# Performance work log

Measured on AMD Instinct MI355X. Metric: run time of the kernel, lower is better.

## Reference

```python
import jax, jax.numpy as jnp
import numpy as np

K = 3
PAD = K // 2
EPS = 1e-5


def setup_inputs() -> dict:
    key = jax.random.key(0)
    k1, k2, k3 = jax.random.split(key, 3)
    B, C, H, W = 16, 256, 56, 56
    x = jax.random.normal(k1, (B, C, H, W), jnp.float32)
    offset = jax.random.normal(k2, (B, 2 * K * K, H, W), jnp.float32)  # matches torch.randn offsets
    weight = jax.random.normal(k3, (C, C, K, K), jnp.float32) * (1.0 / np.sqrt(C * K * K))
    gamma = jnp.ones((C,), jnp.float32)
    beta = jnp.zeros((C,), jnp.float32)
    return {"x": x, "offset": offset, "weight": weight, "gamma": gamma, "beta": beta}


def _bilinear_sample(x, py, px):
    # x: [B,C,H,W]; py,px: [B,H,W] fractional sample coords; zero padding outside.
    B, C, H, W = x.shape
    y0 = jnp.floor(py)
    x0 = jnp.floor(px)
    wy1 = py - y0  # weight for y0+1
    wx1 = px - x0
    wy0 = 1.0 - wy1
    wx0 = 1.0 - wx1
    x_flat = x.reshape(B, C, H * W)

    def corner(yc, xc, w):
        valid = ((yc >= 0) & (yc <= H - 1) & (xc >= 0) & (xc <= W - 1)).astype(x.dtype)
        yi = jnp.clip(yc, 0, H - 1).astype(jnp.int32)
        xi = jnp.clip(xc, 0, W - 1).astype(jnp.int32)
        idx = (yi * W + xi).reshape(B, 1, H * W)
        v = jnp.take_along_axis(x_flat, jnp.broadcast_to(idx, (B, C, H * W)), axis=2)
        return v.reshape(B, C, H, W) * (w * valid)[:, None, :, :]

    return (corner(y0, x0, wy0 * wx0) + corner(y0, x0 + 1, wy0 * wx1)
            + corner(y0 + 1, x0, wy1 * wx0) + corner(y0 + 1, x0 + 1, wy1 * wx1))


def _deform_conv(x, offset, weight):
    B, C, H, W = x.shape
    base_y = jnp.arange(H, dtype=x.dtype)[None, :, None]  # [1,H,1]
    base_x = jnp.arange(W, dtype=x.dtype)[None, None, :]  # [1,1,W]
    out = jnp.zeros((B, weight.shape[0], H, W), x.dtype)
    for k in range(K * K):  # fixed small loop over kernel taps
        kh, kw = k // K, k % K
        py = base_y + (kh - PAD) + offset[:, 2 * k]
        px = base_x + (kw - PAD) + offset[:, 2 * k + 1]
        samp = _bilinear_sample(x, py, px)  # [B,C,H,W]
        out = out + jnp.einsum('bchw,oc->bohw', samp, weight[:, :, kh, kw])
    return out


def reference(x, offset, weight, gamma, beta):
    y = _deform_conv(x, offset, weight)
    mean = y.mean(axis=(0, 2, 3))
    var = y.var(axis=(0, 2, 3))  # biased var, training-mode BN
    yhat = (y - mean[:, None, None]) * jax.lax.rsqrt(var[:, None, None] + EPS)
    return jax.nn.relu(yhat * gamma[:, None, None] + beta[:, None, None])
```

## Files before the change

kernel.cpp:

```cpp
#include <hip/hip_runtime.h>
#include <stdint.h>

#define HW    3136
#define CH    256
#define NBAT  16
#define RDIM  2304
#define NPOS  50176
#define EPSV  1e-5f
#define NCOL  1568

typedef __bf16 bf16x8 __attribute__((ext_vector_type(8)));
typedef float  f32x4  __attribute__((ext_vector_type(4)));
typedef unsigned int u32x4 __attribute__((ext_vector_type(4)));

__device__ __forceinline__ unsigned short f2bf(float f) {
    union { float f; unsigned int u; } z; z.f = f;
    unsigned int u = z.u;
    u += 0x7FFFu + ((u >> 16) & 1u);
    return (unsigned short)(u >> 16);
}

__device__ __forceinline__ unsigned int cvtpk(float lo, float hi) {
    unsigned int r;
    asm("v_cvt_pk_bf16_f32 %0, %1, %2" : "=v"(r) : "v"(lo), "v"(hi));
    return r;
}

__device__ __forceinline__ void gload_lds16(const void* g, void* l) {
    __builtin_amdgcn_global_load_lds(
        (const __attribute__((address_space(1))) unsigned int*)g,
        (__attribute__((address_space(3))) unsigned int*)l,
        16, 0, 0);
}

__global__ __launch_bounds__(256) void k_transpose(const float* __restrict__ x,
                                                   unsigned short* __restrict__ xt) {
    __shared__ float tile[64][65];
    int hw0 = blockIdx.x * 64;
    int c0  = blockIdx.y * 64;
    int b   = blockIdx.z;
    int tx = threadIdx.x & 63;
    int ty = threadIdx.x >> 6;
    const float* xp = x + ((size_t)(b * CH + c0)) * HW + hw0;
#pragma unroll
    for (int i = 0; i < 16; i++) {
        int c_l = ty + i * 4;
        tile[c_l][tx] = xp[(size_t)c_l * HW + tx];
    }
    __syncthreads();
    unsigned short* op = xt + ((size_t)(b * HW + hw0)) * CH + c0;
#pragma unroll
    for (int i = 0; i < 16; i++) {
        int hw_l = ty + i * 4;
        op[(size_t)hw_l * CH + tx] = f2bf(tile[tx][hw_l]);
    }
}

__global__ __launch_bounds__(256) void k_w2(const float* __restrict__ w,
                                            unsigned short* __restrict__ w2) {
    int idx = blockIdx.x * 256 + threadIdx.x;
    int c = idx & 255;
    int k = (idx >> 8) % 9;
    int o = idx / RDIM;
    w2[idx] = f2bf(w[o * RDIM + c * 9 + k]);
}

#define BK 64
__global__ __launch_bounds__(512, 4) void k_fgemm(const unsigned short* __restrict__ xt,
                                                  const float* __restrict__ off,
                                                  const unsigned short* __restrict__ W2,
                                                  float* __restrict__ y,
                                                  float* __restrict__ psum_s,
                                                  float* __restrict__ psum_q) {
    __shared__ __align__(16) unsigned short lA[256 * BK];
    __shared__ __align__(16) unsigned short lB[64 * BK];
    int t    = threadIdx.x;
    int wid  = t >> 6;
    int lane = t & 63;

    int bid  = blockIdx.x;
    int xcd  = bid & 7;
    int j    = bid >> 3;
    int b    = 2 * xcd + (j >= 49 ? 1 : 0);
    int spat = (j >= 49) ? j - 49 : j;
    int n0   = spat * 64;
    const unsigned short* xb = xt + (size_t)b * HW * CH;

    int m_off = (wid >> 1) * 64;
    int n_off = (wid & 1) * 32;
    int fr = lane & 15;
    int fq = lane >> 4;

    int bp  = t >> 3;
    int bcg = t & 7;
    int hw = n0 + bp;
    int h = hw / 56, w = hw - h * 56;
    unsigned short* lbdst = &lB[bp * BK + ((bcg ^ (bp & 7)) * 8)];

    f32x4 acc[4][2];
#pragma unroll
    for (int m = 0; m < 4; m++)
#pragma unroll
        for (int n = 0; n < 2; n++)
            acc[m][n] = (f32x4){0.f, 0.f, 0.f, 0.f};

    for (int tap = 0; tap < 9; tap++) {
        int   cidx[4];
        float cwgt[4];
        {
            float offY = off[((size_t)(b * 18 + 2 * tap)) * HW + hw];
            float offX = off[((size_t)(b * 18 + 2 * tap + 1)) * HW + hw];
            float py = (float)(h + tap / 3 - 1) + offY;
            float px = (float)(w + tap % 3 - 1) + offX;
            float y0f = floorf(py), x0f = floorf(px);
            float fy = py - y0f, fx = px - x0f;
            float wy[2] = {1.f - fy, fy};
            float wx[2] = {1.f - fx, fx};
#pragma unroll
            for (int jj = 0; jj < 4; jj++) {
                int dy = jj >> 1, dx = jj & 1;
                float ycf = y0f + (float)dy, xcf = x0f + (float)dx;
                bool v = (ycf >= 0.f) && (ycf <= 55.f) && (xcf >= 0.f) && (xcf <= 55.f);
                int yi = min(max((int)ycf, 0), 55);
                int xi = min(max((int)xcf, 0), 55);
                cidx[jj] = yi * 56 + xi;
                cwgt[jj] = v ? wy[dy] * wx[dx] : 0.f;
            }
        }

#pragma unroll
        for (int kk4 = 0; kk4 < 4; kk4++) {
            int r0 = tap * 256 + kk4 * 64;
            int c0 = kk4 * 64 + bcg * 8;
            u32x4 cv0 = *(const u32x4*)(xb + (size_t)cidx[0] * CH + c0);
            u32x4 cv1 = *(const u32x4*)(xb + (size_t)cidx[1] * CH + c0);
            u32x4 cv2 = *(const u32x4*)(xb + (size_t)cidx[2] * CH + c0);
            u32x4 cv3 = *(const u32x4*)(xb + (size_t)cidx[3] * CH + c0);
#pragma unroll
            for (int i = 0; i < 4; i++) {
                int q = t + 512 * i;
                int row = q >> 3;
                int part = (q & 7) ^ (row & 7);
                gload_lds16(W2 + (size_t)row * RDIM + r0 + part * 8,
                            &lA[(size_t)(wid * 64 + 512 * i) * 8]);
            }
            {
                float al[4] = {0.f, 0.f, 0.f, 0.f};
                float ah[4] = {0.f, 0.f, 0.f, 0.f};
#pragma unroll
                for (int i = 0; i < 4; i++) {
                    float w0 = cwgt[0], w1 = cwgt[1], w2v = cwgt[2], w3 = cwgt[3];
                    al[i] = fmaf(w0, __uint_as_float(cv0[i] << 16),
                            fmaf(w1, __uint_as_float(cv1[i] << 16),
                            fmaf(w2v, __uint_as_float(cv2[i] << 16),
                                 w3 * __uint_as_float(cv3[i] << 16))));
                    ah[i] = fmaf(w0, __uint_as_float(cv0[i] & 0xffff0000u),
                            fmaf(w1, __uint_as_float(cv1[i] & 0xffff0000u),
                            fmaf(w2v, __uint_as_float(cv2[i] & 0xffff0000u),
                                 w3 * __uint_as_float(cv3[i] & 0xffff0000u))));
                }
                u32x4 ov;
#pragma unroll
                for (int i = 0; i < 4; i++) ov[i] = cvtpk(al[i], ah[i]);
                *(u32x4*)lbdst = ov;
            }
            __syncthreads();
            __builtin_amdgcn_s_setprio(1);
#pragma unroll
            for (int kk = 0; kk < 2; kk++) {
                bf16x8 afr[4], bfr[2];
#pragma unroll
                for (int m = 0; m < 4; m++) {
                    int row = m_off + m * 16 + fr;
                    int slot = (kk * 4 + fq) ^ (row & 7);
                    afr[m] = *(const bf16x8*)&lA[row * BK + slot * 8];
                }
#pragma unroll
                for (int n = 0; n < 2; n++) {
                    int row = n_off + n * 16 + fr;
                    int slot = (kk * 4 + fq) ^ (row & 7);
                    bfr[n] = *(const bf16x8*)&lB[row * BK + slot * 8];
                }
#pragma unroll
                for (int m = 0; m < 4; m++)
#pragma unroll
                    for (int n = 0; n < 2; n++)
                        acc[m][n] = __builtin_amdgcn_mfma_f32_16x16x32_bf16(afr[m], bfr[n], acc[m][n], 0, 0, 0);
            }
            __builtin_amdgcn_s_setprio(0);
            __syncthreads();
        }
    }

    float* yb = y + (size_t)b * CH * HW;
#pragma unroll
    for (int m = 0; m < 4; m++) {
        int o = m_off + m * 16 + fq * 4;
#pragma unroll
        for (int n = 0; n < 2; n++) {
            int p = n0 + n_off + n * 16 + fr;
#pragma unroll
            for (int jj = 0; jj < 4; jj++)
                yb[(size_t)(o + jj) * HW + p] = acc[m][n][jj];
        }
    }

    int blk2 = (b * 49 + spat) * 2 + (wid & 1);
#pragma unroll
    for (int m = 0; m < 4; m++)
#pragma unroll
        for (int jj = 0; jj < 4; jj++) {
            float s = acc[m][0][jj] + acc[m][1][jj];
            float q = acc[m][0][jj] * acc[m][0][jj] + acc[m][1][jj] * acc[m][1][jj];
#pragma unroll
            for (int msk = 1; msk < 16; msk <<= 1) {
                s += __shfl_xor(s, msk);
                q += __shfl_xor(q, msk);
            }
            if (fr == 0) {
                int o = m_off + m * 16 + fq * 4 + jj;
                psum_s[(size_t)o * NCOL + blk2] = s;
                psum_q[(size_t)o * NCOL + blk2] = q;
            }
        }
}

__global__ __launch_bounds__(256) void k_stats2(const float* __restrict__ psum_s,
                                                const float* __restrict__ psum_q,
                                                const float* __restrict__ gamma,
                                                const float* __restrict__ beta,
                                                float* __restrict__ scaleArr,
                                                float* __restrict__ shiftArr) {
    int o = blockIdx.x;
    int t = threadIdx.x;
    float s = 0.f, q = 0.f;
    for (int i = t; i < NCOL; i += 256) {
        s += psum_s[(size_t)o * NCOL + i];
        q += psum_q[(size_t)o * NCOL + i];
    }
    __shared__ float r1[256], r2[256];
    r1[t] = s; r2[t] = q;
    __syncthreads();
    for (int st = 128; st > 0; st >>= 1) {
        if (t < st) { r1[t] += r1[t + st]; r2[t] += r2[t + st]; }
        __syncthreads();
    }
    if (t == 0) {
        float inv = 1.f / (float)NPOS;
        float mean = r1[0] * inv;
        float var  = r2[0] * inv - mean * mean;
        float sc = gamma[o] * rsqrtf(var + EPSV);
        scaleArr[o] = sc;
        shiftArr[o] = beta[o] - mean * sc;
    }
}

__global__ __launch_bounds__(256) void k_norm(float* __restrict__ y,
                                              const float* __restrict__ scaleArr,
                                              const float* __restrict__ shiftArr) {
    const int total4 = NBAT * CH * (HW / 4);
    for (int i = blockIdx.x * 256 + threadIdx.x; i < total4; i += gridDim.x * 256) {
        int o = (i / (HW / 4)) & 255;
        float sc = scaleArr[o], sh = shiftArr[o];
        float4 v = ((const float4*)y)[i];
        float4 r;
        r.x = fmaxf(v.x * sc + sh, 0.f);
        r.y = fmaxf(v.y * sc + sh, 0.f);
        r.z = fmaxf(v.z * sc + sh, 0.f);
        r.w = fmaxf(v.w * sc + sh, 0.f);
        ((float4*)y)[i] = r;
    }
}

extern "C" void kernel_launch(void* const* d_in, const int* in_sizes, int n_in,
                              void* d_out, int out_size, void* d_ws, size_t ws_size,
                              hipStream_t stream) {
    const float* x     = (const float*)d_in[0];
    const float* off   = (const float*)d_in[1];
    const float* wgt   = (const float*)d_in[2];
    const float* gamma = (const float*)d_in[3];
    const float* beta  = (const float*)d_in[4];
    float* out = (float*)d_out;
    char* ws = (char*)d_ws;

    unsigned short* W2 = (unsigned short*)(ws + 0);
    unsigned short* xt = (unsigned short*)(ws + 1179648);
    float* psum_s      = (float*)(ws + 26869760);
    float* psum_q      = (float*)(ws + 28475392);
    float* scaleArr    = (float*)(ws + 30081024);
    float* shiftArr    = (float*)(ws + 30082048);

    k_transpose<<<dim3(49, 4, 16), 256, 0, stream>>>(x, xt);
    k_w2<<<2304, 256, 0, stream>>>(wgt, W2);
    k_fgemm<<<784, 512, 0, stream>>>(xt, off, W2, out, psum_s, psum_q);
    k_stats2<<<256, 256, 0, stream>>>(psum_s, psum_q, gamma, beta, scaleArr, shiftArr);
    k_norm<<<2048, 256, 0, stream>>>(out, scaleArr, shiftArr);
}
```

Measured before the change: 167.8 us.

## Double-buffer LDS tiles and prefetch gathers/offsets one K-step ahead in fused deform GEMM

Converts the fused deformable-conv GEMM main loop into a software-pipelined two-stage schedule. The A (weight) and B (bilinear-sampled activation) LDS tiles are double-buffered. The next step's corner gathers and weight staging are issued before the current MFMA block, and the next tap's offsets are prefetched a tap early. This overlaps global gather latency with matrix math and removes one barrier per step, at the cost of doubling LDS use (80KB per block), which can limit the requested 4 blocks per CU and raise register pressure.

```diff
diff --git a/kernel.cpp b/kernel.cpp
--- a/kernel.cpp
+++ b/kernel.cpp
@@ -72,8 +72,8 @@
                                                   float* __restrict__ y,
                                                   float* __restrict__ psum_s,
                                                   float* __restrict__ psum_q) {
-    __shared__ __align__(16) unsigned short lA[256 * BK];
-    __shared__ __align__(16) unsigned short lB[64 * BK];
+    __shared__ __align__(16) unsigned short lA[2][256 * BK];
+    __shared__ __align__(16) unsigned short lB[2][64 * BK];
     int t    = threadIdx.x;
     int wid  = t >> 6;
     int lane = t & 63;
@@ -95,7 +95,7 @@
     int bcg = t & 7;
     int hw = n0 + bp;
     int h = hw / 56, w = hw - h * 56;
-    unsigned short* lbdst = &lB[bp * BK + ((bcg ^ (bp & 7)) * 8)];
+    int lboff = bp * BK + ((bcg ^ (bp & 7)) * 8);
 
     f32x4 acc[4][2];
 #pragma unroll
@@ -104,92 +104,129 @@
         for (int n = 0; n < 2; n++)
             acc[m][n] = (f32x4){0.f, 0.f, 0.f, 0.f};
 
-    for (int tap = 0; tap < 9; tap++) {
-        int   cidx[4];
-        float cwgt[4];
-        {
-            float offY = off[((size_t)(b * 18 + 2 * tap)) * HW + hw];
-            float offX = off[((size_t)(b * 18 + 2 * tap + 1)) * HW + hw];
-            float py = (float)(h + tap / 3 - 1) + offY;
-            float px = (float)(w + tap % 3 - 1) + offX;
-            float y0f = floorf(py), x0f = floorf(px);
-            float fy = py - y0f, fx = px - x0f;
-            float wy[2] = {1.f - fy, fy};
-            float wx[2] = {1.f - fx, fx};
-#pragma unroll
-            for (int jj = 0; jj < 4; jj++) {
-                int dy = jj >> 1, dx = jj & 1;
-                float ycf = y0f + (float)dy, xcf = x0f + (float)dx;
-                bool v = (ycf >= 0.f) && (ycf <= 55.f) && (xcf >= 0.f) && (xcf <= 55.f);
-                int yi = min(max((int)ycf, 0), 55);
-                int xi = min(max((int)xcf, 0), 55);
-                cidx[jj] = yi * 56 + xi;
-                cwgt[jj] = v ? wy[dy] * wx[dx] : 0.f;
-            }
-        }
-
-#pragma unroll
-        for (int kk4 = 0; kk4 < 4; kk4++) {
-            int r0 = tap * 256 + kk4 * 64;
-            int c0 = kk4 * 64 + bcg * 8;
-            u32x4 cv0 = *(const u32x4*)(xb + (size_t)cidx[0] * CH + c0);
-            u32x4 cv1 = *(const u32x4*)(xb + (size_t)cidx[1] * CH + c0);
-            u32x4 cv2 = *(const u32x4*)(xb + (size_t)cidx[2] * CH + c0);
-            u32x4 cv3 = *(const u32x4*)(xb + (size_t)cidx[3] * CH + c0);
-#pragma unroll
-            for (int i = 0; i < 4; i++) {
-                int q = t + 512 * i;
-                int row = q >> 3;
-                int part = (q & 7) ^ (row & 7);
-                gload_lds16(W2 + (size_t)row * RDIM + r0 + part * 8,
-                            &lA[(size_t)(wid * 64 + 512 * i) * 8]);
-            }
-            {
-                float al[4] = {0.f, 0.f, 0.f, 0.f};
-                float ah[4] = {0.f, 0.f, 0.f, 0.f};
-#pragma unroll
-                for (int i = 0; i < 4; i++) {
-                    float w0 = cwgt[0], w1 = cwgt[1], w2v = cwgt[2], w3 = cwgt[3];
-                    al[i] = fmaf(w0, __uint_as_float(cv0[i] << 16),
-                            fmaf(w1, __uint_as_float(cv1[i] << 16),
-                            fmaf(w2v, __uint_as_float(cv2[i] << 16),
-                                 w3 * __uint_as_float(cv3[i] << 16))));
-                    ah[i] = fmaf(w0, __uint_as_float(cv0[i] & 0xffff0000u),
-                            fmaf(w1, __uint_as_float(cv1[i] & 0xffff0000u),
-                            fmaf(w2v, __uint_as_float(cv2[i] & 0xffff0000u),
-                                 w3 * __uint_as_float(cv3[i] & 0xffff0000u))));
+    int   cidx0, cidx1, cidx2, cidx3;
+    float cwgt0, cwgt1, cwgt2, cwgt3;
+    float offYn, offXn;
+
+#define META_COMPUTE(TAP, OY, OX)                                              \
+    {                                                                          \
+        float py = (float)(h + (TAP) / 3 - 1) + (OY);                          \
+        float px = (float)(w + (TAP) % 3 - 1) + (OX);                          \
+        float y0f = floorf(py), x0f = floorf(px);                              \
+        float fy = py - y0f, fx = px - x0f;                                    \
+        float wy0 = 1.f - fy, wx0 = 1.f - fx;                                  \
+        float ycf0 = y0f, ycf1 = y0f + 1.f, xcf0 = x0f, xcf1 = x0f + 1.f;      \
+        bool vy0 = (ycf0 >= 0.f) && (ycf0 <= 55.f);                            \
+        bool vy1 = (ycf1 >= 0.f) && (ycf1 <= 55.f);                            \
+        bool vx0 = (xcf0 >= 0.f) && (xcf0 <= 55.f);                            \
+        bool vx1 = (xcf1 >= 0.f) && (xcf1 <= 55.f);                            \
+        int yi0 = min(max((int)ycf0, 0), 55), yi1 = min(max((int)ycf1, 0), 55);\
+        int xi0 = min(max((int)xcf0, 0), 55), xi1 = min(max((int)xcf1, 0), 55);\
+        cidx0 = yi0 * 56 + xi0; cwgt0 = (vy0 && vx0) ? wy0 * wx0 : 0.f;        \
+        cidx1 = yi0 * 56 + xi1; cwgt1 = (vy0 && vx1) ? wy0 * fx : 0.f;         \
+        cidx2 = yi1 * 56 + xi0; cwgt2 = (vy1 && vx0) ? fy * wx0 : 0.f;         \
+        cidx3 = yi1 * 56 + xi1; cwgt3 = (vy1 && vx1) ? fy * fx : 0.f;          \
+    }
+
+#define STAGE_A(S, BUF)                                                        \
+    {                                                                          \
+        _Pragma("unroll")                                                      \
+        for (int i = 0; i < 4; i++) {                                          \
+            int q = t + 512 * i;                                               \
+            int row = q >> 3;                                                  \
+            int part = (q & 7) ^ (row & 7);                                    \
+            gload_lds16(W2 + (size_t)row * RDIM + (S) * 64 + part * 8,         \
+                        &lA[BUF][(size_t)(wid * 64 + 512 * i) * 8]);           \
+        }                                                                      \
+    }
+
+#define GATHERS(S)                                                             \
+    {                                                                          \
+        int c0g = ((S) & 3) * 64 + bcg * 8;                                    \
+        nv0 = *(const u32x4*)(xb + (size_t)cidx0 * CH + c0g);                  \
+        nv1 = *(const u32x4*)(xb + (size_t)cidx1 * CH + c0g);                  \
+        nv2 = *(const u32x4*)(xb + (size_t)cidx2 * CH + c0g);                  \
+        nv3 = *(const u32x4*)(xb + (size_t)cidx3 * CH + c0g);                  \
+    }
+
+#define BLEND_WRITE(BUF)                                                       \
+    {                                                                          \
+        float al[4] = {0.f, 0.f, 0.f, 0.f};                                    \
+        float ah[4] = {0.f, 0.f, 0.f, 0.f};                                    \
+        _Pragma("unroll")                                                      \
+        for (int i = 0; i < 4; i++) {                                          \
+            al[i] = fmaf(cwgt0, __uint_as_float(nv0[i] << 16),                 \
+                    fmaf(cwgt1, __uint_as_float(nv1[i] << 16),                 \
+                    fmaf(cwgt2, __uint_as_float(nv2[i] << 16),                 \
+                         cwgt3 * __uint_as_float(nv3[i] << 16))));             \
+            ah[i] = fmaf(cwgt0, __uint_as_float(nv0[i] & 0xffff0000u),         \
+                    fmaf(cwgt1, __uint_as_float(nv1[i] & 0xffff0000u),         \
+                    fmaf(cwgt2, __uint_as_float(nv2[i] & 0xffff0000u),         \
+                         cwgt3 * __uint_as_float(nv3[i] & 0xffff0000u))));     \
+        }                                                                      \
+        u32x4 ov;                                                              \
+        _Pragma("unroll")                                                      \
+        for (int i = 0; i < 4; i++) ov[i] = cvtpk(al[i], ah[i]);               \
+        *(u32x4*)(&lB[BUF][lboff]) = ov;                                       \
+    }
+
+    u32x4 nv0, nv1, nv2, nv3;
+
+    {
+        float oy = off[((size_t)(b * 18 + 0)) * HW + hw];
+        float ox = off[((size_t)(b * 18 + 1)) * HW + hw];
+        META_COMPUTE(0, oy, ox);
+    }
+    GATHERS(0);
+    STAGE_A(0, 0);
+    offYn = off[((size_t)(b * 18 + 2)) * HW + hw];
+    offXn = off[((size_t)(b * 18 + 3)) * HW + hw];
+    BLEND_WRITE(0);
+    __syncthreads();
+
+    for (int s = 0; s < 36; ++s) {
+        int cur = s & 1;
+        int nxt = cur ^ 1;
+        if (s < 35) {
+            int s1 = s + 1;
+            if ((s1 & 3) == 0) {
+                int tap1 = s1 >> 2;
+                META_COMPUTE(tap1, offYn, offXn);
+                if (tap1 < 8) {
+                    offYn = off[((size_t)(b * 18 + 2 * tap1 + 2)) * HW + hw];
+                    offXn = off[((size_t)(b * 18 + 2 * tap1 + 3)) * HW + hw];
                 }
-                u32x4 ov;
-#pragma unroll
-                for (int i = 0; i < 4; i++) ov[i] = cvtpk(al[i], ah[i]);
-                *(u32x4*)lbdst = ov;
-            }
-            __syncthreads();
-            __builtin_amdgcn_s_setprio(1);
-#pragma unroll
-            for (int kk = 0; kk < 2; kk++) {
-                bf16x8 afr[4], bfr[2];
-#pragma unroll
-                for (int m = 0; m < 4; m++) {
-                    int row = m_off + m * 16 + fr;
-                    int slot = (kk * 4 + fq) ^ (row & 7);
-                    afr[m] = *(const bf16x8*)&lA[row * BK + slot * 8];
-                }
-#pragma unroll
-                for (int n = 0; n < 2; n++) {
-                    int row = n_off + n * 16 + fr;
-                    int slot = (kk * 4 + fq) ^ (row & 7);
-                    bfr[n] = *(const bf16x8*)&lB[row * BK + slot * 8];
-                }
-#pragma unroll
-                for (int m = 0; m < 4; m++)
-#pragma unroll
-                    for (int n = 0; n < 2; n++)
-                        acc[m][n] = __builtin_amdgcn_mfma_f32_16x16x32_bf16(afr[m], bfr[n], acc[m][n], 0, 0, 0);
-            }
-            __builtin_amdgcn_s_setprio(0);
-            __syncthreads();
-        }
+            }
+            GATHERS(s1);
+            STAGE_A(s1, nxt);
+        }
+        __builtin_amdgcn_s_setprio(1);
+#pragma unroll
+        for (int kk = 0; kk < 2; kk++) {
+            bf16x8 afr[4], bfr[2];
+#pragma unroll
+            for (int m = 0; m < 4; m++) {
+                int row = m_off + m * 16 + fr;
+                int slot = (kk * 4 + fq) ^ (row & 7);
+                afr[m] = *(const bf16x8*)&lA[cur][row * BK + slot * 8];
+            }
+#pragma unroll
+            for (int n = 0; n < 2; n++) {
+                int row = n_off + n * 16 + fr;
+                int slot = (kk * 4 + fq) ^ (row & 7);
+                bfr[n] = *(const bf16x8*)&lB[cur][row * BK + slot * 8];
+            }
+#pragma unroll
+            for (int m = 0; m < 4; m++)
+#pragma unroll
+                for (int n = 0; n < 2; n++)
+                    acc[m][n] = __builtin_amdgcn_mfma_f32_16x16x32_bf16(afr[m], bfr[n], acc[m][n], 0, 0, 0);
+        }
+        __builtin_amdgcn_s_setprio(0);
+        if (s < 35) {
+            BLEND_WRITE(nxt);
+        }
+        __syncthreads();
     }
 
     float* yb = y + (size_t)b * CH * HW;
```

Result: faster. 164.0 us (-2.2%).
